# Performance work log

Measured on AMD Instinct MI355X. Metric: run time of the kernel, lower is better.

## Reference

```python
import jax, jax.numpy as jnp
from jax import lax
import numpy as np

D_MODEL = 512
D_PROJ = 256
PATCH = 4
NL = 8
D_STATE = 16
D_CONV = 4
EXPAND = 2
D_INNER = EXPAND * D_MODEL          # 1024
DT_RANK = (D_MODEL + 15) // 16      # 32
B = 4
SEQ = 1024
NF = 1
EPS = 1e-5


def setup_inputs() -> dict:
    key = jax.random.key(0)
    ks = jax.random.split(key, 12)
    s = 0.02
    def rn(k, shape):
        return jax.random.normal(k, shape, jnp.float32) * s
    A_init = jnp.log(jnp.arange(1, D_STATE + 1, dtype=jnp.float32))  # (n,)
    return {
        "time_series": jax.random.normal(ks[0], (B, SEQ, NF), jnp.float32),
        "mask": jnp.ones((B, SEQ), jnp.int32),
        "emb_w": rn(ks[1], (D_MODEL, PATCH)),
        "emb_b": jnp.zeros((D_MODEL,), jnp.float32),
        "norm_w": jnp.ones((NL, D_MODEL), jnp.float32),
        "in_w": rn(ks[2], (NL, 2, 2 * D_INNER, D_MODEL)),
        "conv_w": rn(ks[3], (NL, 2, D_INNER, D_CONV)),
        "conv_b": jnp.zeros((NL, 2, D_INNER), jnp.float32),
        "xproj_w": rn(ks[4], (NL, 2, DT_RANK + 2 * D_STATE, D_INNER)),
        "dt_w": rn(ks[5], (NL, 2, D_INNER, DT_RANK)),
        "dt_b": jnp.full((NL, 2, D_INNER), float(np.log(np.expm1(0.01))), jnp.float32),
        "A_log": jnp.broadcast_to(A_init, (NL, 2, D_INNER, D_STATE)) + jnp.zeros((NL, 2, D_INNER, D_STATE), jnp.float32),
        "Dp": jnp.ones((NL, 2, D_INNER), jnp.float32),
        "out_w": rn(ks[6], (NL, 2, D_MODEL, D_INNER)),
        "proj_w": rn(ks[7], (PATCH * D_PROJ, D_MODEL)),
        "proj_b": jnp.zeros((PATCH * D_PROJ,), jnp.float32),
    }


def rmsnorm(x, w):
    return x * lax.rsqrt(jnp.mean(x * x, axis=-1, keepdims=True) + EPS) * w


def mamba(x, in_w, conv_w, conv_b, xproj_w, dt_w, dt_b, A_log, Dp, out_w):
    # x: (B, L, D_MODEL)
    Bsz, L, _ = x.shape
    xz = jnp.einsum('bld,ed->ble', x, in_w)                 # (B,L,2*d_inner)
    u, z = jnp.split(xz, 2, axis=-1)                         # each (B,L,d_inner)
    # depthwise causal conv1d along L
    u_t = jnp.transpose(u, (0, 2, 1))                        # (B,d_inner,L)
    u_pad = jnp.pad(u_t, ((0, 0), (0, 0), (D_CONV - 1, 0)))
    conv = lax.conv_general_dilated(
        u_pad, conv_w[:, None, :], window_strides=(1,), padding='VALID',
        feature_group_count=D_INNER, dimension_numbers=('NCH', 'OIH', 'NCH'))
    u = jax.nn.silu(jnp.transpose(conv + conv_b[None, :, None], (0, 2, 1)))  # (B,L,d_inner)
    x_dbl = jnp.einsum('ble,re->blr', u, xproj_w)            # (B,L,dt_rank+2n)
    dt, Bm, C = jnp.split(x_dbl, [DT_RANK, DT_RANK + D_STATE], axis=-1)
    delta = jax.nn.softplus(jnp.einsum('blr,er->ble', dt, dt_w) + dt_b)  # (B,L,d_inner)
    A = -jnp.exp(A_log)                                      # (d_inner,n)

    def step(h, inp):
        d_t, B_t, C_t, u_t = inp                             # (B,e),(B,n),(B,n),(B,e)
        dA = jnp.exp(d_t[..., None] * A)                     # (B,e,n)
        h = dA * h + (d_t * u_t)[..., None] * B_t[:, None, :]
        y = jnp.einsum('ben,bn->be', h, C_t)
        return h, y

    h0 = jnp.zeros((Bsz, D_INNER, D_STATE), x.dtype)
    xs = (jnp.moveaxis(delta, 1, 0), jnp.moveaxis(Bm, 1, 0),
          jnp.moveaxis(C, 1, 0), jnp.moveaxis(u, 1, 0))
    _, ys = lax.scan(step, h0, xs)                           # ys: (L,B,e)
    y = jnp.moveaxis(ys, 0, 1) + u * Dp
    y = y * jax.nn.silu(z)
    return jnp.einsum('ble,de->bld', y, out_w)               # (B,L,D_MODEL)


def reference(time_series, mask, emb_w, emb_b, norm_w, in_w, conv_w, conv_b,
              xproj_w, dt_w, dt_b, A_log, Dp, out_w, proj_w, proj_b):
    Bsz, S, F_ = time_series.shape
    NP = S // PATCH  # S is a multiple of PATCH
    patches = time_series.reshape(Bsz, NP, PATCH, F_)
    patches = jnp.transpose(patches, (0, 3, 1, 2)).reshape(Bsz, F_ * NP, PATCH)
    x = patches @ emb_w.T + emb_b                            # (B, F*NP, D_MODEL)
    for i in range(NL):
        res = x
        xn = rmsnorm(x, norm_w[i])
        yf = mamba(xn, in_w[i, 0], conv_w[i, 0], conv_b[i, 0], xproj_w[i, 0],
                   dt_w[i, 0], dt_b[i, 0], A_log[i, 0], Dp[i, 0], out_w[i, 0])
        yb = mamba(jnp.flip(xn, axis=1), in_w[i, 1], conv_w[i, 1], conv_b[i, 1],
                   xproj_w[i, 1], dt_w[i, 1], dt_b[i, 1], A_log[i, 1], Dp[i, 1], out_w[i, 1])
        x = yf + jnp.flip(yb, axis=1) + res
    proj = x @ proj_w.T + proj_b                             # (B, F*NP, PATCH*D_PROJ)
    le = proj.reshape(Bsz, F_, NP, PATCH, D_PROJ)
    le = jnp.transpose(le, (0, 2, 3, 1, 4)).reshape(Bsz, NP * PATCH, F_, D_PROJ)
    return le[:, :S]
```

## Files before the change

kernel.cpp:

```cpp
#include <hip/hip_runtime.h>
#include <hip/hip_bf16.h>

#define DM 512
#define DI 1024
#define DSTATE 16
#define DTR 32
#define NLAYER 8
#define BS 4
#define LL 256
#define MT 1024
#define DPROJ 256
#define CL 32
#define NCH (LL/CL)

typedef unsigned short u16;
typedef __attribute__((ext_vector_type(8))) short short8;
typedef __attribute__((ext_vector_type(4))) float f32x4;

__device__ __forceinline__ float sigmoidf_(float x){ return 1.f/(1.f+__expf(-x)); }

__device__ __forceinline__ u16 f2bf(float f){
  unsigned u = __float_as_uint(f);
  u = (u + 0x7FFF + ((u>>16)&1)) >> 16;
  return (u16)u;
}
__device__ __forceinline__ float bf2f(u16 v){
  return __uint_as_float(((unsigned)v) << 16);
}

template<int CTRL>
__device__ __forceinline__ float dpp_ror_add(float x){
  int y = __builtin_amdgcn_update_dpp(0, __float_as_int(x), CTRL, 0xF, 0xF, false);
  return x + __int_as_float(y);
}
__device__ __forceinline__ float sum16_dpp(float x){
  x = dpp_ror_add<0x128>(x);
  x = dpp_ror_add<0x124>(x);
  x = dpp_ror_add<0x122>(x);
  x = dpp_ror_add<0x121>(x);
  return x;
}

__global__ __launch_bounds__(256) void embed_k(const float* __restrict__ ts,
    const float* __restrict__ ew, const float* __restrict__ eb, float* __restrict__ x){
  int idx = blockIdx.x*256 + threadIdx.x;
  int m = idx >> 9, d = idx & 511;
  int b = m >> 8, np_ = m & 255;
  const float* t0 = ts + b*1024 + np_*4;
  float acc = eb[d];
  #pragma unroll
  for (int p=0;p<4;p++) acc = fmaf(t0[p], ew[d*4+p], acc);
  x[idx] = acc;
}

__global__ __launch_bounds__(256) void wcastall_k(
    const float* __restrict__ w_in, const float* __restrict__ w_out,
    const float* __restrict__ w_xp, const float* __restrict__ w_pj,
    u16* __restrict__ dst){
  int t = blockIdx.x*256 + threadIdx.x;
  long e4 = (long)t*4;
  const float* src; long o;
  if      (e4 < 16777216) { src = w_in;  o = e4; }
  else if (e4 < 25165824) { src = w_out; o = e4 - 16777216; }
  else if (e4 < 26214400) { src = w_xp;  o = e4 - 25165824; }
  else                    { src = w_pj;  o = e4 - 26214400; }
  float4 v = *(const float4*)(src + o);
  ushort4 r; r.x=f2bf(v.x); r.y=f2bf(v.y); r.z=f2bf(v.z); r.w=f2bf(v.w);
  *(ushort4*)(dst + e4) = r;
}

__global__ __launch_bounds__(256) void rmscomb_k(float* __restrict__ x,
    const float* __restrict__ yout,
    const float* __restrict__ nw, u16* __restrict__ xnbf, u16* __restrict__ xnfbf){
  int m = blockIdx.x, t = threadIdx.x;
  int b = m>>8, l = m&255, mf = (b<<8)+(255-l);
  float2 v = *(const float2*)&x[(long)m*DM + t*2];
  if (yout){
    float2 f = *(const float2*)&yout[(long)m*DM + t*2];
    float2 g = *(const float2*)&yout[(long)MT*DM + (long)mf*DM + t*2];
    v.x += f.x + g.x; v.y += f.y + g.y;
    *(float2*)&x[(long)m*DM + t*2] = v;
  }
  float ss = v.x*v.x + v.y*v.y;
  ss += __shfl_down(ss,32); ss += __shfl_down(ss,16); ss += __shfl_down(ss,8);
  ss += __shfl_down(ss,4);  ss += __shfl_down(ss,2);  ss += __shfl_down(ss,1);
  __shared__ float ps[4];
  if ((t&63)==0) ps[t>>6] = ss;
  __syncthreads();
  float tot = ps[0]+ps[1]+ps[2]+ps[3];
  float rs = rsqrtf(tot*(1.f/DM) + 1e-5f);
  ushort2 o; o.x = f2bf(v.x*rs*nw[t*2]); o.y = f2bf(v.y*rs*nw[t*2+1]);
  *(ushort2*)&xnbf [(long)m *DM + t*2] = o;
  *(ushort2*)&xnfbf[(long)mf*DM + t*2] = o;
}

__global__ __launch_bounds__(256) void combcast_k(const float* __restrict__ x,
    const float* __restrict__ yout, u16* __restrict__ xbf){
  int idx = blockIdx.x*256 + threadIdx.x;
  int m = idx >> 7, c4 = idx & 127;
  int b = m>>8, l = m&255, mf = (b<<8)+(255-l);
  float4 r = ((const float4*)x)[idx];
  float4 f = ((const float4*)yout)[idx];
  float4 g = ((const float4*)(yout + (long)MT*DM))[(long)mf*128 + c4];
  ushort4 o;
  o.x = f2bf(r.x + f.x + g.x); o.y = f2bf(r.y + f.y + g.y);
  o.z = f2bf(r.z + f.z + g.z); o.w = f2bf(r.w + f.w + g.w);
  ((ushort4*)xbf)[idx] = o;
}

template<int BM,int BN,int SPLITK,int EPI>
__global__ __launch_bounds__(256) void mfma_nt(
    const u16* __restrict__ A, int lda, long sA,
    const u16* __restrict__ W, int ldw, long sW,
    const float* __restrict__ bias,
    float* __restrict__ C, int ldc, long sC,
    int M, int N, int K)
{
  constexpr int WM = BM/2, WN = BN/2;
  constexpr int MI = WM/16, NI = WN/16;
  int z = blockIdx.z;
  int dir = z / SPLITK, kc = z % SPLITK;
  int Klen = K / SPLITK;
  int kbase = kc * Klen;
  A += (long)dir * sA;
  W += (long)dir * sW;
  if (SPLITK > 1) C += (long)z * M * N; else C += (long)dir * sC;

  __shared__ u16 Al[BM*32];
  __shared__ u16 Wl[BN*32];
  int tid = threadIdx.x;
  int lane = tid & 63;
  int wave = tid >> 6;
  int wm0 = (wave>>1)*WM, wn0 = (wave&1)*WN;
  int m0 = blockIdx.y*BM, n0 = blockIdx.x*BN;
  int l16 = lane>>4, l15 = lane&15;

  f32x4 acc[MI][NI] = {};

  for (int k0=0; k0<Klen; k0+=32){
    #pragma unroll
    for (int it=0; it<BM*4/256; ++it){
      int ch = it*256 + tid;
      int row = ch % BM, kk = ch / BM;
      const u16* g = A + (long)(m0+row)*lda + kbase + k0 + kk*8;
      __builtin_amdgcn_global_load_lds(
          (const __attribute__((address_space(1))) void*)g,
          (__attribute__((address_space(3))) void*)(Al + ch*8), 16, 0, 0);
    }
    #pragma unroll
    for (int it=0; it<BN*4/256; ++it){
      int ch = it*256 + tid;
      int row = ch % BN, kk = ch / BN;
      const u16* g = W + (long)(n0+row)*ldw + kbase + k0 + kk*8;
      __builtin_amdgcn_global_load_lds(
          (const __attribute__((address_space(1))) void*)g,
          (__attribute__((address_space(3))) void*)(Wl + ch*8), 16, 0, 0);
    }
    __syncthreads();
    short8 a[MI], b[NI];
    #pragma unroll
    for (int i=0;i<MI;i++)
      a[i] = *(const short8*)&Al[(l16*BM + wm0 + i*16 + l15)*8];
    #pragma unroll
    for (int j=0;j<NI;j++)
      b[j] = *(const short8*)&Wl[(l16*BN + wn0 + j*16 + l15)*8];
    #pragma unroll
    for (int i=0;i<MI;i++)
      #pragma unroll
      for (int j=0;j<NI;j++)
        acc[i][j] = __builtin_amdgcn_mfma_f32_16x16x32_bf16(a[i], b[j], acc[i][j], 0,0,0);
    __syncthreads();
  }
  #pragma unroll
  for (int i=0;i<MI;i++){
    #pragma unroll
    for (int j=0;j<NI;j++){
      #pragma unroll
      for (int r=0;r<4;r++){
        int m = m0 + wm0 + i*16 + l16*4 + r;
        int n = n0 + wn0 + j*16 + l15;
        float v = acc[i][j][r];
        if (EPI==2){
          v += bias[n];
          int bb = m>>8, np_ = m&255, p = n>>8, dp = n&255;
          C[((long)(bb*1024 + np_*4 + p))*256 + dp] = v;
        } else {
          C[(long)m*ldc + n] = v;
        }
      }
    }
  }
}

__global__ __launch_bounds__(256) void xreduce_k(const float* __restrict__ part,
    float* __restrict__ xdbl){
  int idx = blockIdx.x*256 + threadIdx.x;
  int d = idx >> 16, off = idx & 65535;
  float s = 0.f;
  #pragma unroll
  for (int kc=0; kc<8; ++kc) s += part[((d*8+kc)<<16) + off];
  xdbl[idx] = s;
}

__global__ __launch_bounds__(256) void conv_silu_k(const float* __restrict__ xz,
    const float* __restrict__ cw, const float* __restrict__ cb,
    u16* __restrict__ ubf){
  int idx = blockIdx.x*256 + threadIdx.x;
  int e = idx & (DI-1);
  int grp = idx >> 10;
  int dir = grp >> 8;
  int b   = (grp >> 6) & 3;
  int l0  = (grp & 63) * 4;
  long dm0 = (long)dir*MT + b*LL + l0;
  const float* w = cw + ((long)dir*DI + e)*4;
  float w0=w[0], w1=w[1], w2=w[2], w3=w[3];
  float bias = cb[dir*DI + e];
  const float* src = xz + dm0*2048 + e;
  float vb[7];
  #pragma unroll
  for (int j=0;j<7;j++){
    int l = l0 - 3 + j;
    vb[j] = (l >= 0) ? src[(long)(j-3)*2048] : 0.f;
  }
  #pragma unroll
  for (int j=0;j<4;j++){
    float acc = bias;
    acc = fmaf(w0, vb[j],   acc);
    acc = fmaf(w1, vb[j+1], acc);
    acc = fmaf(w2, vb[j+2], acc);
    acc = fmaf(w3, vb[j+3], acc);
    float v = acc * sigmoidf_(acc);
    ubf[(dm0+j)*DI + e] = f2bf(v);
  }
}

__global__ __launch_bounds__(256) void scan_k(
    const u16* __restrict__ ubf, const float* __restrict__ xz,
    const float* __restrict__ xdbl, const float* __restrict__ dtw,
    const float* __restrict__ dtb, const float* __restrict__ A_log,
    const float* __restrict__ Dp, u16* __restrict__ ygbf)
{
  int t = threadIdx.x;
  int n = t & 15, el = t >> 4;
  int ec = blockIdx.x, b = blockIdx.y, dir = blockIdx.z;
  int e0 = ec*16, e = e0 + el;
  float Av = -__expf(A_log[((long)dir*DI + e)*16 + n]);
  float Dv = Dp[dir*DI + e];
  long mbase = (long)dir*MT + b*LL;
  const u16*  up_ = ubf + mbase*DI;
  const float* zp_ = xz + mbase*2048 + 1024;
  const float* xd_ = xdbl + mbase*64;
  u16* yp_ = ygbf + mbase*DI;

  float wrow[32];
  {
    const float* wr = dtw + ((long)dir*DI + e0 + n)*32;
    #pragma unroll
    for (int r4=0;r4<8;r4++) *(float4*)&wrow[r4*4] = *(const float4*)&wr[r4*4];
  }
  float dtbv = dtb[dir*DI + e0 + n];

  __shared__ float sdt[2][CL][32];
  __shared__ float sBC[2][CL][32];
  __shared__ float sU [2][CL][16];
  __shared__ float sD [CL][16];
  __shared__ float sy [CL][16];

  float4 xv0, xv1; ushort4 uvv;
  auto load_pre = [&](int c){
    long l0 = (long)c*CL;
    int f0 = t, f1 = t + 256;
    xv0 = *(const float4*)&xd_[(l0 + (f0>>4))*64 + (f0&15)*4];
    xv1 = *(const float4*)&xd_[(l0 + (f1>>4))*64 + (f1&15)*4];
    if (t < 128) uvv = *(const ushort4*)&up_[(l0 + (t>>2))*DI + e0 + (t&3)*4];
  };
  auto write_pre = [&](int buf){
    {
      int row = t>>4, c4 = (t&15)*4;
      if (c4 < 32) *(float4*)&sdt[buf][row][c4] = xv0;
      else         *(float4*)&sBC[buf][row][c4-32] = xv0;
    }
    {
      int f1 = t + 256;
      int row = f1>>4, c4 = (f1&15)*4;
      if (c4 < 32) *(float4*)&sdt[buf][row][c4] = xv1;
      else         *(float4*)&sBC[buf][row][c4-32] = xv1;
    }
    if (t < 128){
      float4 uf;
      uf.x = bf2f(uvv.x); uf.y = bf2f(uvv.y); uf.z = bf2f(uvv.z); uf.w = bf2f(uvv.w);
      *(float4*)&sU[buf][t>>2][(t&3)*4] = uf;
    }
  };

  load_pre(0);
  write_pre(0);
  load_pre(1);
  __syncthreads();

  float h = 0.f;
  for (int c = 0; c < NCH; ++c){
    int cur = c & 1;
    #pragma unroll
    for (int j=0;j<2;j++){
      int l = (t>>4)*2 + j;
      float acc = dtbv;
      #pragma unroll
      for (int r4=0;r4<8;r4++){
        float4 d4 = *(const float4*)&sdt[cur][l][r4*4];
        acc = fmaf(d4.x, wrow[r4*4],   acc);
        acc = fmaf(d4.y, wrow[r4*4+1], acc);
        acc = fmaf(d4.z, wrow[r4*4+2], acc);
        acc = fmaf(d4.w, wrow[r4*4+3], acc);
      }
      acc = (acc>20.f) ? acc : log1pf(__expf(acc));
      sD[l][n] = acc;
    }
    float4 zc;
    if (t < 128) zc = *(const float4*)&zp_[((long)c*CL + (t>>2))*2048 + e0 + (t&3)*4];
    __syncthreads();

    const float* pD  = &sD[0][el];
    const float* pU  = &sU[cur][0][el];
    const float* pBC = &sBC[cur][0][n];
    #pragma unroll
    for (int c8 = 0; c8 < 4; ++c8){
      const float* pD8  = pD  + c8*128;
      const float* pU8  = pU  + c8*128;
      const float* pBC8 = pBC + c8*256;
      #pragma unroll
      for (int l8 = 0; l8 < 8; ++l8){
        float dv = pD8[l8*16];
        float uv = pU8[l8*16];
        float Bv = pBC8[l8*32], Cv = pBC8[l8*32 + 16];
        float dA = __expf(dv*Av);
        h = fmaf(dA, h, dv*uv*Bv);
        float yc = sum16_dpp(h*Cv);
        if (n==0) sy[c8*8+l8][el] = yc + uv*Dv;
      }
    }
    __syncthreads();
    if (c+1 < NCH){
      write_pre(cur^1);
      if (c+2 < NCH) load_pre(c+2);
    }
    if (t < 128){
      float4 y4 = *(const float4*)&sy[t>>2][(t&3)*4];
      float gx = zc.x*sigmoidf_(zc.x), gy = zc.y*sigmoidf_(zc.y);
      float gz = zc.z*sigmoidf_(zc.z), gw = zc.w*sigmoidf_(zc.w);
      ushort4 o; o.x=f2bf(y4.x*gx); o.y=f2bf(y4.y*gy); o.z=f2bf(y4.z*gz); o.w=f2bf(y4.w*gw);
      *(ushort4*)&yp_[((long)c*CL + (t>>2))*DI + e0 + (t&3)*4] = o;
    }
    __syncthreads();
  }
}

extern "C" void kernel_launch(void* const* d_in, const int* in_sizes, int n_in,
                              void* d_out, int out_size, void* d_ws, size_t ws_size,
                              hipStream_t stream){
  const float* ts   = (const float*)d_in[0];
  const float* ew   = (const float*)d_in[2];
  const float* eb   = (const float*)d_in[3];
  const float* nw   = (const float*)d_in[4];
  const float* inw  = (const float*)d_in[5];
  const float* cw   = (const float*)d_in[6];
  const float* cb   = (const float*)d_in[7];
  const float* xpw  = (const float*)d_in[8];
  const float* dtw  = (const float*)d_in[9];
  const float* dtb  = (const float*)d_in[10];
  const float* alog = (const float*)d_in[11];
  const float* dpp  = (const float*)d_in[12];
  const float* outw = (const float*)d_in[13];
  const float* pw   = (const float*)d_in[14];
  const float* pb   = (const float*)d_in[15];
  float* out = (float*)d_out;

  float* ws   = (float*)d_ws;
  float* x    = ws;
  float* xz   = ws + 524288;
  float* xdbl = ws + 4718592;
  float* yout = ws + 4849664;
  float* xpart= ws + 5898240;
  u16* ub     = (u16*)(ws + 6946816);
  u16* xn_bf  = ub;
  u16* u_bf   = ub + 1048576;
  u16* yg_bf  = ub + 3145728;
  u16* x_bf   = ub + 5242880;
  u16* wb     = ub + 5767168;
  u16* wb_in  = wb;
  u16* wb_out = wb + 16777216;
  u16* wb_xp  = wb + 25165824;
  u16* wb_pj  = wb + 26214400;

  dim3 blk(256);

  embed_k<<<MT*DM/256, blk, 0, stream>>>(ts, ew, eb, x);
  wcastall_k<<<26112, blk, 0, stream>>>(inw, outw, xpw, pw, wb);

  for (int i=0;i<NLAYER;i++){
    rmscomb_k<<<MT, blk, 0, stream>>>(x, i ? yout : nullptr, nw + i*DM,
        xn_bf, xn_bf + MT*DM);
    mfma_nt<64,128,1,0><<<dim3(16,16,2), blk, 0, stream>>>(
        xn_bf, DM, (long)MT*DM, wb_in + (long)i*2097152, DM, 1048576,
        nullptr, xz, 2048, (long)MT*2048, MT, 2048, DM);
    conv_silu_k<<<2048, blk, 0, stream>>>(xz, cw + (long)i*2*DI*4, cb + i*2*DI, u_bf);
    mfma_nt<64,64,8,0><<<dim3(1,16,16), blk, 0, stream>>>(
        u_bf, DI, (long)MT*DI, wb_xp + (long)i*131072, DI, 65536,
        nullptr, xpart, 64, 0, MT, 64, DI);
    xreduce_k<<<512, blk, 0, stream>>>(xpart, xdbl);
    scan_k<<<dim3(64, BS, 2), blk, 0, stream>>>(u_bf, xz, xdbl,
        dtw + (long)i*2*DI*DTR, dtb + (long)i*2*DI,
        alog + (long)i*2*DI*16, dpp + i*2*DI, yg_bf);
    mfma_nt<64,64,1,0><<<dim3(8,16,2), blk, 0, stream>>>(
        yg_bf, DI, (long)MT*DI, wb_out + (long)i*1048576, DI, 524288,
        nullptr, yout, DM, (long)MT*DM, MT, DM, DI);
  }
  combcast_k<<<MT*DM/4/256, blk, 0, stream>>>(x, yout, x_bf);
  mfma_nt<64,64,1,2><<<dim3(16,16,1), blk, 0, stream>>>(
      x_bf, DM, 0, wb_pj, DM, 0, pb, out, 1024, 0, MT, 1024, DM);
}
```

Baseline: 796.8 us.

## Fuse SiLU gate into in-projection epilogue as bf16; pad scan shared arrays

Result: faster. 766.4 us (-3.8%).

```diff
diff --git a/kernel.cpp b/kernel.cpp
--- a/kernel.cpp
+++ b/kernel.cpp
@@ -12,6 +12,7 @@
 #define DPROJ 256
 #define CL 32
 #define NCH (LL/CL)
+#define SP 20
 
 typedef unsigned short u16;
 typedef __attribute__((ext_vector_type(8))) short short8;
@@ -112,7 +113,7 @@
 __global__ __launch_bounds__(256) void mfma_nt(
     const u16* __restrict__ A, int lda, long sA,
     const u16* __restrict__ W, int ldw, long sW,
-    const float* __restrict__ bias,
+    const float* __restrict__ bias, u16* __restrict__ G,
     float* __restrict__ C, int ldc, long sC,
     int M, int N, int K)
 {
@@ -125,6 +126,7 @@
   A += (long)dir * sA;
   W += (long)dir * sW;
   if (SPLITK > 1) C += (long)z * M * N; else C += (long)dir * sC;
+  if (EPI==4) G += (long)dir * (long)MT*DI;
 
   __shared__ u16 Al[BM*32];
   __shared__ u16 Wl[BN*32];
@@ -184,6 +186,9 @@
           v += bias[n];
           int bb = m>>8, np_ = m&255, p = n>>8, dp = n&255;
           C[((long)(bb*1024 + np_*4 + p))*256 + dp] = v;
+        } else if (EPI==4){
+          if (n < 1024) C[(long)m*1024 + n] = v;
+          else          G[(long)m*1024 + (n-1024)] = f2bf(v * sigmoidf_(v));
         } else {
           C[(long)m*ldc + n] = v;
         }
@@ -202,7 +207,7 @@
   xdbl[idx] = s;
 }
 
-__global__ __launch_bounds__(256) void conv_silu_k(const float* __restrict__ xz,
+__global__ __launch_bounds__(256) void conv_silu_k(const float* __restrict__ xzu,
     const float* __restrict__ cw, const float* __restrict__ cb,
     u16* __restrict__ ubf){
   int idx = blockIdx.x*256 + threadIdx.x;
@@ -215,12 +220,12 @@
   const float* w = cw + ((long)dir*DI + e)*4;
   float w0=w[0], w1=w[1], w2=w[2], w3=w[3];
   float bias = cb[dir*DI + e];
-  const float* src = xz + dm0*2048 + e;
+  const float* src = xzu + dm0*DI + e;
   float vb[7];
   #pragma unroll
   for (int j=0;j<7;j++){
     int l = l0 - 3 + j;
-    vb[j] = (l >= 0) ? src[(long)(j-3)*2048] : 0.f;
+    vb[j] = (l >= 0) ? src[(long)(j-3)*DI] : 0.f;
   }
   #pragma unroll
   for (int j=0;j<4;j++){
@@ -235,7 +240,7 @@
 }
 
 __global__ __launch_bounds__(256) void scan_k(
-    const u16* __restrict__ ubf, const float* __restrict__ xz,
+    const u16* __restrict__ ubf, const u16* __restrict__ gbf,
     const float* __restrict__ xdbl, const float* __restrict__ dtw,
     const float* __restrict__ dtb, const float* __restrict__ A_log,
     const float* __restrict__ Dp, u16* __restrict__ ygbf)
@@ -247,8 +252,8 @@
   float Av = -__expf(A_log[((long)dir*DI + e)*16 + n]);
   float Dv = Dp[dir*DI + e];
   long mbase = (long)dir*MT + b*LL;
-  const u16*  up_ = ubf + mbase*DI;
-  const float* zp_ = xz + mbase*2048 + 1024;
+  const u16* up_ = ubf + mbase*DI;
+  const u16* gp_ = gbf + mbase*DI;
   const float* xd_ = xdbl + mbase*64;
   u16* yp_ = ygbf + mbase*DI;
 
@@ -262,9 +267,9 @@
 
   __shared__ float sdt[2][CL][32];
   __shared__ float sBC[2][CL][32];
-  __shared__ float sU [2][CL][16];
-  __shared__ float sD [CL][16];
-  __shared__ float sy [CL][16];
+  __shared__ float sU [2][CL][SP];
+  __shared__ float sD [CL][SP];
+  __shared__ float sy [CL][SP];
 
   float4 xv0, xv1; ushort4 uvv;
   auto load_pre = [&](int c){
@@ -313,11 +318,11 @@
         acc = fmaf(d4.z, wrow[r4*4+2], acc);
         acc = fmaf(d4.w, wrow[r4*4+3], acc);
       }
-      acc = (acc>20.f) ? acc : log1pf(__expf(acc));
+      acc = fmaxf(acc, 0.f) + __logf(1.f + __expf(-fabsf(acc)));
       sD[l][n] = acc;
     }
-    float4 zc;
-    if (t < 128) zc = *(const float4*)&zp_[((long)c*CL + (t>>2))*2048 + e0 + (t&3)*4];
+    ushort4 gv;
+    if (t < 128) gv = *(const ushort4*)&gp_[((long)c*CL + (t>>2))*DI + e0 + (t&3)*4];
     __syncthreads();
 
     const float* pD  = &sD[0][el];
@@ -325,13 +330,13 @@
     const float* pBC = &sBC[cur][0][n];
     #pragma unroll
     for (int c8 = 0; c8 < 4; ++c8){
-      const float* pD8  = pD  + c8*128;
-      const float* pU8  = pU  + c8*128;
+      const float* pD8  = pD  + c8*8*SP;
+      const float* pU8  = pU  + c8*8*SP;
       const float* pBC8 = pBC + c8*256;
       #pragma unroll
       for (int l8 = 0; l8 < 8; ++l8){
-        float dv = pD8[l8*16];
-        float uv = pU8[l8*16];
+        float dv = pD8[l8*SP];
+        float uv = pU8[l8*SP];
         float Bv = pBC8[l8*32], Cv = pBC8[l8*32 + 16];
         float dA = __expf(dv*Av);
         h = fmaf(dA, h, dv*uv*Bv);
@@ -346,9 +351,9 @@
     }
     if (t < 128){
       float4 y4 = *(const float4*)&sy[t>>2][(t&3)*4];
-      float gx = zc.x*sigmoidf_(zc.x), gy = zc.y*sigmoidf_(zc.y);
-      float gz = zc.z*sigmoidf_(zc.z), gw = zc.w*sigmoidf_(zc.w);
-      ushort4 o; o.x=f2bf(y4.x*gx); o.y=f2bf(y4.y*gy); o.z=f2bf(y4.z*gz); o.w=f2bf(y4.w*gw);
+      ushort4 o;
+      o.x = f2bf(y4.x * bf2f(gv.x)); o.y = f2bf(y4.y * bf2f(gv.y));
+      o.z = f2bf(y4.z * bf2f(gv.z)); o.w = f2bf(y4.w * bf2f(gv.w));
       *(ushort4*)&yp_[((long)c*CL + (t>>2))*DI + e0 + (t&3)*4] = o;
     }
     __syncthreads();
@@ -377,16 +382,17 @@
 
   float* ws   = (float*)d_ws;
   float* x    = ws;
-  float* xz   = ws + 524288;
-  float* xdbl = ws + 4718592;
-  float* yout = ws + 4849664;
-  float* xpart= ws + 5898240;
-  u16* ub     = (u16*)(ws + 6946816);
+  float* xzu  = ws + 524288;
+  float* xdbl = ws + 2621440;
+  float* yout = ws + 2752512;
+  float* xpart= ws + 3801088;
+  u16* ub     = (u16*)(ws + 4849664);
   u16* xn_bf  = ub;
   u16* u_bf   = ub + 1048576;
-  u16* yg_bf  = ub + 3145728;
-  u16* x_bf   = ub + 5242880;
-  u16* wb     = ub + 5767168;
+  u16* g_bf   = ub + 3145728;
+  u16* yg_bf  = ub + 5242880;
+  u16* x_bf   = ub + 7340032;
+  u16* wb     = ub + 7864320;
   u16* wb_in  = wb;
   u16* wb_out = wb + 16777216;
   u16* wb_xp  = wb + 25165824;
@@ -400,22 +406,22 @@
   for (int i=0;i<NLAYER;i++){
     rmscomb_k<<<MT, blk, 0, stream>>>(x, i ? yout : nullptr, nw + i*DM,
         xn_bf, xn_bf + MT*DM);
-    mfma_nt<64,128,1,0><<<dim3(16,16,2), blk, 0, stream>>>(
+    mfma_nt<64,128,1,4><<<dim3(16,16,2), blk, 0, stream>>>(
         xn_bf, DM, (long)MT*DM, wb_in + (long)i*2097152, DM, 1048576,
-        nullptr, xz, 2048, (long)MT*2048, MT, 2048, DM);
-    conv_silu_k<<<2048, blk, 0, stream>>>(xz, cw + (long)i*2*DI*4, cb + i*2*DI, u_bf);
+        nullptr, g_bf, xzu, 1024, (long)MT*1024, MT, 2048, DM);
+    conv_silu_k<<<2048, blk, 0, stream>>>(xzu, cw + (long)i*2*DI*4, cb + i*2*DI, u_bf);
     mfma_nt<64,64,8,0><<<dim3(1,16,16), blk, 0, stream>>>(
         u_bf, DI, (long)MT*DI, wb_xp + (long)i*131072, DI, 65536,
-        nullptr, xpart, 64, 0, MT, 64, DI);
+        nullptr, nullptr, xpart, 64, 0, MT, 64, DI);
     xreduce_k<<<512, blk, 0, stream>>>(xpart, xdbl);
-    scan_k<<<dim3(64, BS, 2), blk, 0, stream>>>(u_bf, xz, xdbl,
+    scan_k<<<dim3(64, BS, 2), blk, 0, stream>>>(u_bf, g_bf, xdbl,
         dtw + (long)i*2*DI*DTR, dtb + (long)i*2*DI,
         alog + (long)i*2*DI*16, dpp + i*2*DI, yg_bf);
     mfma_nt<64,64,1,0><<<dim3(8,16,2), blk, 0, stream>>>(
         yg_bf, DI, (long)MT*DI, wb_out + (long)i*1048576, DI, 524288,
-        nullptr, yout, DM, (long)MT*DM, MT, DM, DI);
+        nullptr, nullptr, yout, DM, (long)MT*DM, MT, DM, DI);
   }
   combcast_k<<<MT*DM/4/256, blk, 0, stream>>>(x, yout, x_bf);
   mfma_nt<64,64,1,2><<<dim3(16,16,1), blk, 0, stream>>>(
-      x_bf, DM, 0, wb_pj, DM, 0, pb, out, 1024, 0, MT, 1024, DM);
-}
+      x_bf, DM, 0, wb_pj, DM, 0, pb, nullptr, out, 1024, 0, MT, 1024, DM);
+}
```
